# Optimization experiments

Hardware: AMD Instinct MI355X
Metric: run time of the kernel (lower is better)

## Reference

```python
import jax, jax.numpy as jnp
import numpy as np
from jax import lax

NUM_BINS = 64
GROUP = 16
HIDDEN = 128
DOWNSAMPLE = 32
EPS = 1e-6


def _conv2d(x, w, b, pad, groups=1):
    # x: (N, Cin, H, W), w: (Cout, Cin//groups, kh, kw)
    y = lax.conv_general_dilated(
        x, w, window_strides=(1, 1), padding=[(pad, pad), (pad, pad)],
        dimension_numbers=("NCHW", "OIHW", "NCHW"), feature_group_count=groups)
    return y + b[None, :, None, None]


def _lut_net(delta_cdf, w1, b1, w2, b2, w3, b3):
    # MonotonicLUT1D.forward on (1, G, 1, K)
    h = jax.nn.relu(_conv2d(delta_cdf, w1, b1, pad=2))
    h = jax.nn.relu(_conv2d(h, w2, b2, pad=2, groups=HIDDEN))
    d = _conv2d(h, w3, b3, pad=0)
    d = jax.nn.softplus(d)
    cdf = jnp.cumsum(d, axis=-1)
    cdf = cdf / (cdf[..., -1:] + EPS)
    identity = jnp.linspace(0.0, 1.0, NUM_BINS, dtype=cdf.dtype).reshape(1, 1, 1, -1)
    return cdf + identity  # (1, G, 1, K)


def reference(x, w1, b1, w2, b2, w3, b3, alpha):
    B, C, H, W = x.shape
    K, G, ds = NUM_BINS, GROUP, DOWNSAMPLE

    # per-sample, per-channel min-max normalize
    x_min = jnp.min(x, axis=(2, 3), keepdims=True)
    x_max = jnp.max(x, axis=(2, 3), keepdims=True)
    x01 = (x - x_min) / (x_max - x_min + EPS)

    # exact adaptive avg pool to (ds, ds) (H, W divisible by ds)
    x_small = x01.reshape(B, C, ds, H // ds, ds, W // ds).mean(axis=(3, 5))
    x_small = lax.stop_gradient(x_small)  # detach_hist=True

    # histogram CDF estimate (no grad in original)
    x_group = x_small.reshape(B, G, C // G, ds, ds).mean(axis=2)  # (B, G, ds, ds)
    idx = jnp.clip(jnp.round(x_group * (K - 1)).astype(jnp.int32), 0, K - 1)
    idx = idx.reshape(B, G, -1)
    hist = jax.nn.one_hot(idx, K, dtype=jnp.float32).sum(axis=2)  # (B, G, K)
    pdf = hist / (hist.sum(axis=-1, keepdims=True) + EPS)
    cdf = jnp.cumsum(pdf, axis=-1)
    delta_cdf = cdf.mean(axis=0, keepdims=True).reshape(1, G, 1, K).astype(x.dtype)

    adapt_cdf = _lut_net(delta_cdf, w1, b1, w2, b2, w3, b3)  # (1, G, 1, K)

    # per-pixel LUT gather + lerp
    lut = adapt_cdf[0, :, 0, :]                 # (G, K)
    group_ids = jnp.arange(C) // (C // G)
    lut_c = lut[group_ids]                       # (C, K)

    pos = x01 * (K - 1)
    idx_lo = jnp.clip(jnp.floor(pos).astype(jnp.int32), 0, K - 1)
    idx_hi = jnp.clip(idx_lo + 1, 0, K - 1)
    w_hi = (pos - idx_lo).astype(lut.dtype)

    lut_e = jnp.broadcast_to(lut_c[None], (B, C, K))
    v_lo = jnp.take_along_axis(lut_e, idx_lo.reshape(B, C, -1), axis=2)
    v_hi = jnp.take_along_axis(lut_e, idx_hi.reshape(B, C, -1), axis=2)
    x_eq01 = (v_lo + w_hi.reshape(B, C, -1) * (v_hi - v_lo)).reshape(B, C, H, W)

    a = jax.nn.sigmoid(alpha)
    out01 = a * x_eq01 + (1.0 - a) * x01
    return out01 * (x_max - x_min) + x_min


def setup_inputs() -> dict:
    key = jax.random.key(0)
    ks = jax.random.split(key, 8)
    B, C, H, W = 2, 16, 1024, 1024
    x = jax.random.normal(ks[0], (B, C, H, W), dtype=jnp.float32)
    w1 = jax.random.normal(ks[1], (HIDDEN, GROUP, 5, 5), dtype=jnp.float32) * 0.05
    b1 = jnp.zeros((HIDDEN,), dtype=jnp.float32)
    w2 = jax.random.normal(ks[2], (HIDDEN, 1, 5, 5), dtype=jnp.float32) * 0.05
    b2 = jnp.zeros((HIDDEN,), dtype=jnp.float32)
    w3 = jax.random.normal(ks[3], (GROUP, HIDDEN, 1, 1), dtype=jnp.float32) * 0.05
    b3 = jnp.zeros((GROUP,), dtype=jnp.float32)
    alpha = jnp.asarray(0.25, dtype=jnp.float32)
    return {"x": x, "w1": w1, "b1": b1, "w2": w2, "b2": b2, "w3": w3, "b3": b3, "alpha": alpha}
```

## Files before the change

kernel.cpp:

```cpp
#include <hip/hip_runtime.h>
#include <math.h>

#define NBINS   64
#define GROUPS  16
#define HIDDEN  128
#define EPSF    1e-6f

#define IMG_ELEMS   (1024*1024)
#define F4_PER_ROW  256
#define NIMG        32

typedef float nfloat4 __attribute__((ext_vector_type(4)));

__global__ __launch_bounds__(256) void k_stats(
        const float* __restrict__ x,
        float* __restrict__ blocksum,
        float* __restrict__ pmin,
        float* __restrict__ pmax)
{
    const int bid = blockIdx.x;
    const int bc  = bid >> 5;
    const int i   = bid & 31;
    const int t   = threadIdx.x;
    const int lane = t & 63;
    const int wave = t >> 6;

    const float4* xin = (const float4*)(x + (size_t)bc * IMG_ELEMS);
    const int rowbase = (i * 32) * F4_PER_ROW;

    float s = 0.f, mn = INFINITY, mx = -INFINITY;
    #pragma unroll 4
    for (int r = 0; r < 32; ++r) {
        float4 v = xin[rowbase + r * F4_PER_ROW + t];
        s += (v.x + v.y) + (v.z + v.w);
        mn = fminf(mn, fminf(fminf(v.x, v.y), fminf(v.z, v.w)));
        mx = fmaxf(mx, fmaxf(fmaxf(v.x, v.y), fmaxf(v.z, v.w)));
    }

    s += __shfl_xor(s, 4, 64);
    s += __shfl_xor(s, 2, 64);
    s += __shfl_xor(s, 1, 64);
    if ((t & 7) == 0)
        blocksum[bc * 1024 + i * 32 + (t >> 3)] = s;

    #pragma unroll
    for (int st = 32; st > 0; st >>= 1) {
        mn = fminf(mn, __shfl_xor(mn, st, 64));
        mx = fmaxf(mx, __shfl_xor(mx, st, 64));
    }
    __shared__ float wmn[4], wmx[4];
    if (lane == 0) { wmn[wave] = mn; wmx[wave] = mx; }
    __syncthreads();
    if (t == 0) {
        pmin[bid] = fminf(fminf(wmn[0], wmn[1]), fminf(wmn[2], wmn[3]));
        pmax[bid] = fmaxf(fmaxf(wmx[0], wmx[1]), fmaxf(wmx[2], wmx[3]));
    }
}

__global__ __launch_bounds__(256) void k_hist(
        const float* __restrict__ pmin, const float* __restrict__ pmax,
        const float* __restrict__ blocksum,
        float* __restrict__ gmin, float* __restrict__ gmax,
        float* __restrict__ pcdf)
{
    const int bc   = blockIdx.x;
    const int t    = threadIdx.x;
    const int lane = t & 63;
    const int wave = t >> 6;

    __shared__ float s_mn, s_inv;
    if (wave == 0) {
        float mn = (lane < 32) ? pmin[bc * 32 + lane] : INFINITY;
        float mx = (lane < 32) ? pmax[bc * 32 + lane] : -INFINITY;
        #pragma unroll
        for (int st = 32; st > 0; st >>= 1) {
            mn = fminf(mn, __shfl_xor(mn, st, 64));
            mx = fmaxf(mx, __shfl_xor(mx, st, 64));
        }
        if (lane == 0) {
            gmin[bc] = mn; gmax[bc] = mx;
            s_mn = mn; s_inv = 1.0f / (mx - mn + EPSF);
        }
    }
    __syncthreads();
    const float mnv = s_mn;
    const float inv = s_inv;

    int idx0, idx1, idx2, idx3;
    {
        const float* bs = blocksum + bc * 1024;
        #define MKIDX(D, IT) { \
            float bmean = bs[t + (IT)*256] * (1.0f / 1024.0f); \
            float xs = (bmean - mnv) * inv; \
            int id = (int)rintf(xs * 63.0f); \
            D = max(0, min(id, 63)); }
        MKIDX(idx0, 0) MKIDX(idx1, 1) MKIDX(idx2, 2) MKIDX(idx3, 3)
        #undef MKIDX
    }

    int cnt = 0;
    #pragma unroll 1
    for (int b = 0; b < NBINS; ++b) {
        unsigned long long m0 = __ballot(idx0 == b);
        unsigned long long m1 = __ballot(idx1 == b);
        unsigned long long m2 = __ballot(idx2 == b);
        unsigned long long m3 = __ballot(idx3 == b);
        int p = __popcll(m0) + __popcll(m1) + __popcll(m2) + __popcll(m3);
        cnt += (lane == b) ? p : 0;
    }

    __shared__ int whist[4][NBINS];
    whist[wave][lane] = cnt;
    __syncthreads();

    if (t < NBINS) {
        int h = whist[0][t] + whist[1][t] + whist[2][t] + whist[3][t];
        #pragma unroll
        for (int d = 1; d < 64; d <<= 1) {
            int v = __shfl_up(h, d, 64);
            if (t >= d) h += v;
        }
        const float scale = 0.5f / (1024.0f + EPSF);
        pcdf[bc * NBINS + t] = (float)h * scale;
    }
}

__global__ __launch_bounds__(256) void k_conv12(
        const float* __restrict__ pcdf,
        const float* __restrict__ w1, const float* __restrict__ b1,
        const float* __restrict__ w2, const float* __restrict__ b2,
        float* __restrict__ h2)
{
    __shared__ float dcdf[GROUPS][NBINS];
    __shared__ float w1s[4 * GROUPS * 5];
    __shared__ float w2s[4][5];
    __shared__ float h1s[4][NBINS + 4];

    const int t   = threadIdx.x;
    const int ocb = blockIdx.x * 4;
    const int ocl = t >> 6;
    const int k   = t & 63;

    for (int o = t; o < GROUPS * NBINS; o += 256)
        ((float*)dcdf)[o] = pcdf[o] + pcdf[GROUPS * NBINS + o];

    for (int o = t; o < 4 * GROUPS * 5; o += 256) {
        const int oo  = o / 80;
        const int rem = o - oo * 80;
        const int ic  = rem / 5;
        const int tap = rem - ic * 5;
        w1s[o] = w1[((ocb + oo) * GROUPS + ic) * 25 + 10 + tap];
    }
    if (t < 20) w2s[t / 5][t % 5] = w2[(ocb + t / 5) * 25 + 10 + t % 5];
    if (t < 4)  { h1s[t][0] = 0.f; h1s[t][1] = 0.f;
                  h1s[t][NBINS + 2] = 0.f; h1s[t][NBINS + 3] = 0.f; }
    __syncthreads();

    float acc = b1[ocb + ocl];
    const float* wrow = w1s + ocl * 80;
    for (int ic = 0; ic < GROUPS; ++ic) {
        #pragma unroll
        for (int tap = 0; tap < 5; ++tap) {
            const int kk = k - 2 + tap;
            if (kk >= 0 && kk < NBINS)
                acc += wrow[ic * 5 + tap] * dcdf[ic][kk];
        }
    }
    h1s[ocl][k + 2] = fmaxf(acc, 0.f);
    __syncthreads();

    float a = b2[ocb + ocl];
    #pragma unroll
    for (int tap = 0; tap < 5; ++tap)
        a += w2s[ocl][tap] * h1s[ocl][k + tap];
    h2[(ocb + ocl) * NBINS + k] = fmaxf(a, 0.f);
}

__global__ __launch_bounds__(256) void k_tail(
        const float* __restrict__ h2,
        const float* __restrict__ w3, const float* __restrict__ b3,
        float* __restrict__ lut)
{
    __shared__ float h2s[HIDDEN][NBINS];
    __shared__ float w3s[GROUPS * HIDDEN];
    __shared__ float sd[GROUPS][NBINS];
    const int t = threadIdx.x;

    for (int o = t; o < HIDDEN * NBINS; o += 256) ((float*)h2s)[o] = h2[o];
    for (int o = t; o < GROUPS * HIDDEN; o += 256) w3s[o] = w3[o];
    __syncthreads();

    const int k = t & 63;
    const int g0 = t >> 6;
    float acc0 = b3[g0 + 0];
    float acc1 = b3[g0 + 4];
    float acc2 = b3[g0 + 8];
    float acc3 = b3[g0 + 12];
    for (int h = 0; h < HIDDEN; ++h) {
        const float v = h2s[h][k];
        acc0 += w3s[(g0 + 0) * HIDDEN + h] * v;
        acc1 += w3s[(g0 + 4) * HIDDEN + h] * v;
        acc2 += w3s[(g0 + 8) * HIDDEN + h] * v;
        acc3 += w3s[(g0 + 12) * HIDDEN + h] * v;
    }
    #define SOFTPLUS(z) (fmaxf(z, 0.f) + log1pf(expf(-fabsf(z))))
    sd[g0 + 0][k]  = SOFTPLUS(acc0);
    sd[g0 + 4][k]  = SOFTPLUS(acc1);
    sd[g0 + 8][k]  = SOFTPLUS(acc2);
    sd[g0 + 12][k] = SOFTPLUS(acc3);
    #undef SOFTPLUS
    __syncthreads();

    if (t < GROUPS) {
        float run = 0.f;
        for (int kk = 0; kk < NBINS; ++kk) { run += sd[t][kk]; sd[t][kk] = run; }
        const float invn = 1.0f / (run + EPSF);
        for (int kk = 0; kk < NBINS; ++kk)
            lut[t * NBINS + kk] = sd[t][kk] * invn + (float)kk * (1.0f / 63.0f);
    }
}

__device__ __forceinline__ float remap1(float v, float mnv, float inv, float r,
                                        float aa, const float* lut_s)
{
    float x01 = (v - mnv) * inv;
    float pos = x01 * 63.0f;
    int il = (int)floorf(pos);
    il = max(0, min(il, 63));
    const int ih = min(il + 1, 63);
    const float w = pos - (float)il;
    const float vlo = lut_s[il];
    const float vhi = lut_s[ih];
    const float xe = fmaf(w, vhi - vlo, vlo);
    const float o01 = aa * xe + (1.0f - aa) * x01;
    return o01 * r + mnv;
}

__global__ __launch_bounds__(256) void k_apply(
        const float* __restrict__ x,
        const float* __restrict__ gmin, const float* __restrict__ gmax,
        const float* __restrict__ lut, const float* __restrict__ alpha,
        float* __restrict__ out)
{
    const int img  = blockIdx.x >> 6;
    const int part = blockIdx.x & 63;
    const int c    = img & 15;
    const int t    = threadIdx.x;

    __shared__ float lut_s[NBINS];
    if (t < NBINS) lut_s[t] = lut[c * NBINS + t];
    __syncthreads();

    const float mnv = gmin[img];
    const float mxv = gmax[img];
    const float r   = mxv - mnv;
    const float inv = 1.0f / (r + EPSF);
    const float aa  = 1.0f / (1.0f + expf(-alpha[0]));

    const size_t base4 = (size_t)img * (IMG_ELEMS / 4) + (size_t)part * 4096;
    const float4* xin = (const float4*)x;
    nfloat4* o4 = (nfloat4*)out;

    #pragma unroll 2
    for (int it = 0; it < 16; ++it) {
        const size_t f = base4 + (size_t)t + (size_t)it * 256;
        float4 v = xin[f];
        nfloat4 w;
        w.x = remap1(v.x, mnv, inv, r, aa, lut_s);
        w.y = remap1(v.y, mnv, inv, r, aa, lut_s);
        w.z = remap1(v.z, mnv, inv, r, aa, lut_s);
        w.w = remap1(v.w, mnv, inv, r, aa, lut_s);
        __builtin_nontemporal_store(w, &o4[f]);
    }
}

extern "C" void kernel_launch(void* const* d_in, const int* in_sizes, int n_in,
                              void* d_out, int out_size, void* d_ws, size_t ws_size,
                              hipStream_t stream)
{
    const float* x     = (const float*)d_in[0];
    const float* w1    = (const float*)d_in[1];
    const float* b1    = (const float*)d_in[2];
    const float* w2    = (const float*)d_in[3];
    const float* b2    = (const float*)d_in[4];
    const float* w3    = (const float*)d_in[5];
    const float* b3    = (const float*)d_in[6];
    const float* alpha = (const float*)d_in[7];
    float* out = (float*)d_out;

    float* ws = (float*)d_ws;
    float* blocksum = ws;
    float* pmin     = ws + 32768;
    float* pmax     = ws + 33792;
    float* gmin     = ws + 34816;
    float* gmax     = ws + 34848;
    float* lut      = ws + 34880;
    float* pcdf     = ws + 35904;
    float* h2       = ws + 37952;

    k_stats <<<NIMG * 32, 256, 0, stream>>>(x, blocksum, pmin, pmax);
    k_hist  <<<NIMG,      256, 0, stream>>>(pmin, pmax, blocksum, gmin, gmax, pcdf);
    k_conv12<<<32,        256, 0, stream>>>(pcdf, w1, b1, w2, b2, h2);
    k_tail  <<<1,         256, 0, stream>>>(h2, w3, b3, lut);
    k_apply <<<NIMG * 64, 256, 0, stream>>>(x, gmin, gmax, lut, alpha, out);
}
```

Before: 88.03 us.

## Fuse histogram, conv and LUT-tail kernels into one single-block kernel

The three small middle kernels (per-image histogram/CDF, the two conv layers, and the 1x1 conv with softplus/cumsum tail) are merged into one 1024-thread, single-block kernel. Every intermediate (pcdf, h1/h2) now stays in shared memory, which removes two kernel launches and the global round-trips between them. In exchange, work that used to spread across 32 blocks now runs serially on a single CU, including eight sequential histogram iterations per team. The second conv also updates h1 in place within a wave, relying on lockstep execution with no barrier.

Result: slower. 258.3 us, median of 2 (+193.5%).

```diff
diff --git a/kernel.cpp b/kernel.cpp
--- a/kernel.cpp
+++ b/kernel.cpp
@@ -57,158 +57,118 @@
     }
 }
 
-__global__ __launch_bounds__(256) void k_hist(
+__global__ __launch_bounds__(1024) void k_mid(
         const float* __restrict__ pmin, const float* __restrict__ pmax,
         const float* __restrict__ blocksum,
+        const float* __restrict__ w1, const float* __restrict__ b1,
+        const float* __restrict__ w2, const float* __restrict__ b2,
+        const float* __restrict__ w3, const float* __restrict__ b3,
         float* __restrict__ gmin, float* __restrict__ gmax,
-        float* __restrict__ pcdf)
-{
-    const int bc   = blockIdx.x;
+        float* __restrict__ lut)
+{
     const int t    = threadIdx.x;
     const int lane = t & 63;
     const int wave = t >> 6;
 
-    __shared__ float s_mn, s_inv;
-    if (wave == 0) {
-        float mn = (lane < 32) ? pmin[bc * 32 + lane] : INFINITY;
-        float mx = (lane < 32) ? pmax[bc * 32 + lane] : -INFINITY;
+    __shared__ float s_mn[NIMG], s_inv[NIMG];
+    __shared__ float pcdf_l[NIMG][NBINS];
+    __shared__ int   whist[4][4][NBINS];
+    __shared__ float dcdf[GROUPS][NBINS];
+    __shared__ float h1[HIDDEN][NBINS];
+    __shared__ float sd[GROUPS][NBINS];
+
+    {
+        const int pair = t >> 5, j = t & 31;
+        float mn = pmin[pair * 32 + j];
+        float mx = pmax[pair * 32 + j];
         #pragma unroll
-        for (int st = 32; st > 0; st >>= 1) {
+        for (int st = 16; st > 0; st >>= 1) {
             mn = fminf(mn, __shfl_xor(mn, st, 64));
             mx = fmaxf(mx, __shfl_xor(mx, st, 64));
         }
-        if (lane == 0) {
-            gmin[bc] = mn; gmax[bc] = mx;
-            s_mn = mn; s_inv = 1.0f / (mx - mn + EPSF);
-        }
-    }
-    __syncthreads();
-    const float mnv = s_mn;
-    const float inv = s_inv;
-
-    int idx0, idx1, idx2, idx3;
-    {
+        if (j == 0) {
+            gmin[pair] = mn; gmax[pair] = mx;
+            s_mn[pair] = mn; s_inv[pair] = 1.0f / (mx - mn + EPSF);
+        }
+    }
+    __syncthreads();
+
+    const int team = wave >> 2;
+    const int q    = wave & 3;
+    const int lt   = q * 64 + lane;
+    for (int iter = 0; iter < 8; ++iter) {
+        const int bc = team * 8 + iter;
+        const float mnv = s_mn[bc];
+        const float inv = s_inv[bc];
         const float* bs = blocksum + bc * 1024;
-        #define MKIDX(D, IT) { \
-            float bmean = bs[t + (IT)*256] * (1.0f / 1024.0f); \
-            float xs = (bmean - mnv) * inv; \
-            int id = (int)rintf(xs * 63.0f); \
-            D = max(0, min(id, 63)); }
-        MKIDX(idx0, 0) MKIDX(idx1, 1) MKIDX(idx2, 2) MKIDX(idx3, 3)
-        #undef MKIDX
-    }
-
-    int cnt = 0;
-    #pragma unroll 1
-    for (int b = 0; b < NBINS; ++b) {
-        unsigned long long m0 = __ballot(idx0 == b);
-        unsigned long long m1 = __ballot(idx1 == b);
-        unsigned long long m2 = __ballot(idx2 == b);
-        unsigned long long m3 = __ballot(idx3 == b);
-        int p = __popcll(m0) + __popcll(m1) + __popcll(m2) + __popcll(m3);
-        cnt += (lane == b) ? p : 0;
-    }
-
-    __shared__ int whist[4][NBINS];
-    whist[wave][lane] = cnt;
-    __syncthreads();
-
-    if (t < NBINS) {
-        int h = whist[0][t] + whist[1][t] + whist[2][t] + whist[3][t];
+        int idx[4];
         #pragma unroll
-        for (int d = 1; d < 64; d <<= 1) {
-            int v = __shfl_up(h, d, 64);
-            if (t >= d) h += v;
-        }
-        const float scale = 0.5f / (1024.0f + EPSF);
-        pcdf[bc * NBINS + t] = (float)h * scale;
-    }
-}
-
-__global__ __launch_bounds__(256) void k_conv12(
-        const float* __restrict__ pcdf,
-        const float* __restrict__ w1, const float* __restrict__ b1,
-        const float* __restrict__ w2, const float* __restrict__ b2,
-        float* __restrict__ h2)
-{
-    __shared__ float dcdf[GROUPS][NBINS];
-    __shared__ float w1s[4 * GROUPS * 5];
-    __shared__ float w2s[4][5];
-    __shared__ float h1s[4][NBINS + 4];
-
-    const int t   = threadIdx.x;
-    const int ocb = blockIdx.x * 4;
-    const int ocl = t >> 6;
-    const int k   = t & 63;
-
-    for (int o = t; o < GROUPS * NBINS; o += 256)
-        ((float*)dcdf)[o] = pcdf[o] + pcdf[GROUPS * NBINS + o];
-
-    for (int o = t; o < 4 * GROUPS * 5; o += 256) {
-        const int oo  = o / 80;
-        const int rem = o - oo * 80;
-        const int ic  = rem / 5;
-        const int tap = rem - ic * 5;
-        w1s[o] = w1[((ocb + oo) * GROUPS + ic) * 25 + 10 + tap];
-    }
-    if (t < 20) w2s[t / 5][t % 5] = w2[(ocb + t / 5) * 25 + 10 + t % 5];
-    if (t < 4)  { h1s[t][0] = 0.f; h1s[t][1] = 0.f;
-                  h1s[t][NBINS + 2] = 0.f; h1s[t][NBINS + 3] = 0.f; }
-    __syncthreads();
-
-    float acc = b1[ocb + ocl];
-    const float* wrow = w1s + ocl * 80;
-    for (int ic = 0; ic < GROUPS; ++ic) {
+        for (int i = 0; i < 4; ++i) {
+            float bmean = bs[lt + i * 256] * (1.0f / 1024.0f);
+            float xs = (bmean - mnv) * inv;
+            int id = (int)rintf(xs * 63.0f);
+            idx[i] = max(0, min(id, 63));
+        }
+        int cnt = 0;
+        #pragma unroll 1
+        for (int b = 0; b < NBINS; ++b) {
+            int p = __popcll(__ballot(idx[0] == b)) + __popcll(__ballot(idx[1] == b))
+                  + __popcll(__ballot(idx[2] == b)) + __popcll(__ballot(idx[3] == b));
+            cnt += (lane == b) ? p : 0;
+        }
+        whist[team][q][lane] = cnt;
+        __syncthreads();
+        if (q == 0) {
+            int h = whist[team][0][lane] + whist[team][1][lane]
+                  + whist[team][2][lane] + whist[team][3][lane];
+            #pragma unroll
+            for (int d = 1; d < 64; d <<= 1) {
+                int v = __shfl_up(h, d, 64);
+                if (lane >= d) h += v;
+            }
+            pcdf_l[bc][lane] = (float)h * (0.5f / (1024.0f + EPSF));
+        }
+        __syncthreads();
+    }
+
+    dcdf[wave][lane] = pcdf_l[wave][lane] + pcdf_l[GROUPS + wave][lane];
+    __syncthreads();
+
+    for (int i = 0; i < 8; ++i) {
+        const int oc = i * 16 + wave;
+        const int k  = lane;
+        float acc = b1[oc];
+        const float* wp = w1 + (oc * GROUPS) * 25 + 10;
+        for (int ic = 0; ic < GROUPS; ++ic) {
+            const float* wrow = wp + ic * 25;
+            #pragma unroll
+            for (int tap = 0; tap < 5; ++tap) {
+                const int kk = k - 2 + tap;
+                if (kk >= 0 && kk < NBINS)
+                    acc += wrow[tap] * dcdf[ic][kk];
+            }
+        }
+        h1[oc][k] = fmaxf(acc, 0.f);
+        const float* w2p = w2 + oc * 25 + 10;
+        float a = b2[oc];
         #pragma unroll
         for (int tap = 0; tap < 5; ++tap) {
             const int kk = k - 2 + tap;
             if (kk >= 0 && kk < NBINS)
-                acc += wrow[ic * 5 + tap] * dcdf[ic][kk];
-        }
-    }
-    h1s[ocl][k + 2] = fmaxf(acc, 0.f);
-    __syncthreads();
-
-    float a = b2[ocb + ocl];
-    #pragma unroll
-    for (int tap = 0; tap < 5; ++tap)
-        a += w2s[ocl][tap] * h1s[ocl][k + tap];
-    h2[(ocb + ocl) * NBINS + k] = fmaxf(a, 0.f);
-}
-
-__global__ __launch_bounds__(256) void k_tail(
-        const float* __restrict__ h2,
-        const float* __restrict__ w3, const float* __restrict__ b3,
-        float* __restrict__ lut)
-{
-    __shared__ float h2s[HIDDEN][NBINS];
-    __shared__ float w3s[GROUPS * HIDDEN];
-    __shared__ float sd[GROUPS][NBINS];
-    const int t = threadIdx.x;
-
-    for (int o = t; o < HIDDEN * NBINS; o += 256) ((float*)h2s)[o] = h2[o];
-    for (int o = t; o < GROUPS * HIDDEN; o += 256) w3s[o] = w3[o];
-    __syncthreads();
-
-    const int k = t & 63;
-    const int g0 = t >> 6;
-    float acc0 = b3[g0 + 0];
-    float acc1 = b3[g0 + 4];
-    float acc2 = b3[g0 + 8];
-    float acc3 = b3[g0 + 12];
-    for (int h = 0; h < HIDDEN; ++h) {
-        const float v = h2s[h][k];
-        acc0 += w3s[(g0 + 0) * HIDDEN + h] * v;
-        acc1 += w3s[(g0 + 4) * HIDDEN + h] * v;
-        acc2 += w3s[(g0 + 8) * HIDDEN + h] * v;
-        acc3 += w3s[(g0 + 12) * HIDDEN + h] * v;
-    }
-    #define SOFTPLUS(z) (fmaxf(z, 0.f) + log1pf(expf(-fabsf(z))))
-    sd[g0 + 0][k]  = SOFTPLUS(acc0);
-    sd[g0 + 4][k]  = SOFTPLUS(acc1);
-    sd[g0 + 8][k]  = SOFTPLUS(acc2);
-    sd[g0 + 12][k] = SOFTPLUS(acc3);
-    #undef SOFTPLUS
+                a += w2p[tap] * h1[oc][kk];
+        }
+        h1[oc][k] = fmaxf(a, 0.f);
+    }
+    __syncthreads();
+
+    {
+        const int g = wave, k = lane;
+        float acc = b3[g];
+        const float* w3p = w3 + g * HIDDEN;
+        for (int h = 0; h < HIDDEN; ++h)
+            acc += w3p[h] * h1[h][k];
+        sd[g][k] = fmaxf(acc, 0.f) + log1pf(expf(-fabsf(acc)));
+    }
     __syncthreads();
 
     if (t < GROUPS) {
@@ -295,12 +255,10 @@
     float* gmin     = ws + 34816;
     float* gmax     = ws + 34848;
     float* lut      = ws + 34880;
-    float* pcdf     = ws + 35904;
-    float* h2       = ws + 37952;
-
-    k_stats <<<NIMG * 32, 256, 0, stream>>>(x, blocksum, pmin, pmax);
-    k_hist  <<<NIMG,      256, 0, stream>>>(pmin, pmax, blocksum, gmin, gmax, pcdf);
-    k_conv12<<<32,        256, 0, stream>>>(pcdf, w1, b1, w2, b2, h2);
-    k_tail  <<<1,         256, 0, stream>>>(h2, w3, b3, lut);
-    k_apply <<<NIMG * 64, 256, 0, stream>>>(x, gmin, gmax, lut, alpha, out);
-}
+
+    k_stats<<<NIMG * 32, 256,  0, stream>>>(x, blocksum, pmin, pmax);
+    k_mid  <<<1,         1024, 0, stream>>>(pmin, pmax, blocksum,
+                                            w1, b1, w2, b2, w3, b3,
+                                            gmin, gmax, lut);
+    k_apply<<<NIMG * 64, 256,  0, stream>>>(x, gmin, gmax, lut, alpha, out);
+}
```

## Fuse LUT tail into apply kernel and use shuffles for depthwise conv

Applied to the files above, without the earlier changes.

Removes the single-block k_tail kernel by having every k_apply block recompute its channel's 1x1 conv, softplus, cumsum and normalisation into shared memory. The depthwise conv in k_conv12 now reads neighbours through wavefront shuffles instead of a shared buffer and an extra barrier. This saves one serial launch and a low-occupancy kernel on the critical path. In exchange, each of the 2048 apply blocks redoes a 128x64 dot-product reduction plus a shuffle scan before streaming its pixels.

After: 81.93 us. -6.9%, faster.

```diff
diff --git a/kernel.cpp b/kernel.cpp
--- a/kernel.cpp
+++ b/kernel.cpp
@@ -134,7 +134,6 @@
     __shared__ float dcdf[GROUPS][NBINS];
     __shared__ float w1s[4 * GROUPS * 5];
     __shared__ float w2s[4][5];
-    __shared__ float h1s[4][NBINS + 4];
 
     const int t   = threadIdx.x;
     const int ocb = blockIdx.x * 4;
@@ -152,8 +151,6 @@
         w1s[o] = w1[((ocb + oo) * GROUPS + ic) * 25 + 10 + tap];
     }
     if (t < 20) w2s[t / 5][t % 5] = w2[(ocb + t / 5) * 25 + 10 + t % 5];
-    if (t < 4)  { h1s[t][0] = 0.f; h1s[t][1] = 0.f;
-                  h1s[t][NBINS + 2] = 0.f; h1s[t][NBINS + 3] = 0.f; }
     __syncthreads();
 
     float acc = b1[ocb + ocl];
@@ -166,89 +163,61 @@
                 acc += wrow[ic * 5 + tap] * dcdf[ic][kk];
         }
     }
-    h1s[ocl][k + 2] = fmaxf(acc, 0.f);
-    __syncthreads();
-
+    const float c1 = fmaxf(acc, 0.f);
+
+    const float m2 = __shfl_up(c1, 2, 64);
+    const float m1 = __shfl_up(c1, 1, 64);
+    const float p1 = __shfl_down(c1, 1, 64);
+    const float p2 = __shfl_down(c1, 2, 64);
     float a = b2[ocb + ocl];
-    #pragma unroll
-    for (int tap = 0; tap < 5; ++tap)
-        a += w2s[ocl][tap] * h1s[ocl][k + tap];
+    a += w2s[ocl][0] * ((k >= 2) ? m2 : 0.f);
+    a += w2s[ocl][1] * ((k >= 1) ? m1 : 0.f);
+    a += w2s[ocl][2] * c1;
+    a += w2s[ocl][3] * ((k <= 62) ? p1 : 0.f);
+    a += w2s[ocl][4] * ((k <= 61) ? p2 : 0.f);
     h2[(ocb + ocl) * NBINS + k] = fmaxf(a, 0.f);
-}
-
-__global__ __launch_bounds__(256) void k_tail(
-        const float* __restrict__ h2,
-        const float* __restrict__ w3, const float* __restrict__ b3,
-        float* __restrict__ lut)
-{
-    __shared__ float h2s[HIDDEN][NBINS];
-    __shared__ float w3s[GROUPS * HIDDEN];
-    __shared__ float sd[GROUPS][NBINS];
-    const int t = threadIdx.x;
-
-    for (int o = t; o < HIDDEN * NBINS; o += 256) ((float*)h2s)[o] = h2[o];
-    for (int o = t; o < GROUPS * HIDDEN; o += 256) w3s[o] = w3[o];
-    __syncthreads();
-
-    const int k = t & 63;
-    const int g0 = t >> 6;
-    float acc0 = b3[g0 + 0];
-    float acc1 = b3[g0 + 4];
-    float acc2 = b3[g0 + 8];
-    float acc3 = b3[g0 + 12];
-    for (int h = 0; h < HIDDEN; ++h) {
-        const float v = h2s[h][k];
-        acc0 += w3s[(g0 + 0) * HIDDEN + h] * v;
-        acc1 += w3s[(g0 + 4) * HIDDEN + h] * v;
-        acc2 += w3s[(g0 + 8) * HIDDEN + h] * v;
-        acc3 += w3s[(g0 + 12) * HIDDEN + h] * v;
-    }
-    #define SOFTPLUS(z) (fmaxf(z, 0.f) + log1pf(expf(-fabsf(z))))
-    sd[g0 + 0][k]  = SOFTPLUS(acc0);
-    sd[g0 + 4][k]  = SOFTPLUS(acc1);
-    sd[g0 + 8][k]  = SOFTPLUS(acc2);
-    sd[g0 + 12][k] = SOFTPLUS(acc3);
-    #undef SOFTPLUS
-    __syncthreads();
-
-    if (t < GROUPS) {
-        float run = 0.f;
-        for (int kk = 0; kk < NBINS; ++kk) { run += sd[t][kk]; sd[t][kk] = run; }
-        const float invn = 1.0f / (run + EPSF);
-        for (int kk = 0; kk < NBINS; ++kk)
-            lut[t * NBINS + kk] = sd[t][kk] * invn + (float)kk * (1.0f / 63.0f);
-    }
-}
-
-__device__ __forceinline__ float remap1(float v, float mnv, float inv, float r,
-                                        float aa, const float* lut_s)
-{
-    float x01 = (v - mnv) * inv;
-    float pos = x01 * 63.0f;
-    int il = (int)floorf(pos);
-    il = max(0, min(il, 63));
-    const int ih = min(il + 1, 63);
-    const float w = pos - (float)il;
-    const float vlo = lut_s[il];
-    const float vhi = lut_s[ih];
-    const float xe = fmaf(w, vhi - vlo, vlo);
-    const float o01 = aa * xe + (1.0f - aa) * x01;
-    return o01 * r + mnv;
 }
 
 __global__ __launch_bounds__(256) void k_apply(
         const float* __restrict__ x,
         const float* __restrict__ gmin, const float* __restrict__ gmax,
-        const float* __restrict__ lut, const float* __restrict__ alpha,
+        const float* __restrict__ h2,
+        const float* __restrict__ w3, const float* __restrict__ b3,
+        const float* __restrict__ alpha,
         float* __restrict__ out)
 {
     const int img  = blockIdx.x >> 6;
     const int part = blockIdx.x & 63;
     const int c    = img & 15;
     const int t    = threadIdx.x;
-
+    const int q    = t >> 6;
+    const int k    = t & 63;
+
+    __shared__ float partial[4][NBINS];
     __shared__ float lut_s[NBINS];
-    if (t < NBINS) lut_s[t] = lut[c * NBINS + t];
+
+    {
+        float part_acc = 0.f;
+        const float* w3p = w3 + c * HIDDEN + q * 32;
+        const float* h2p = h2 + (q * 32) * NBINS + k;
+        #pragma unroll 8
+        for (int h = 0; h < 32; ++h)
+            part_acc += w3p[h] * h2p[h * NBINS];
+        partial[q][k] = part_acc;
+    }
+    __syncthreads();
+    if (q == 0) {
+        float acc = b3[c] + ((partial[0][k] + partial[1][k])
+                           + (partial[2][k] + partial[3][k]));
+        float d = fmaxf(acc, 0.f) + log1pf(expf(-fabsf(acc)));
+        #pragma unroll
+        for (int dd = 1; dd < 64; dd <<= 1) {
+            float v = __shfl_up(d, dd, 64);
+            if (k >= dd) d += v;
+        }
+        const float tot = __shfl(d, 63, 64);
+        lut_s[k] = d / (tot + EPSF) + (float)k * (1.0f / 63.0f);
+    }
     __syncthreads();
 
     const float mnv = gmin[img];
@@ -266,10 +235,42 @@
         const size_t f = base4 + (size_t)t + (size_t)it * 256;
         float4 v = xin[f];
         nfloat4 w;
-        w.x = remap1(v.x, mnv, inv, r, aa, lut_s);
-        w.y = remap1(v.y, mnv, inv, r, aa, lut_s);
-        w.z = remap1(v.z, mnv, inv, r, aa, lut_s);
-        w.w = remap1(v.w, mnv, inv, r, aa, lut_s);
+        {
+            float x01 = (v.x - mnv) * inv;
+            float pos = x01 * 63.0f;
+            int il = max(0, min((int)floorf(pos), 63));
+            int ih = min(il + 1, 63);
+            float wt = pos - (float)il;
+            float vlo = lut_s[il], vhi = lut_s[ih];
+            w.x = (aa * fmaf(wt, vhi - vlo, vlo) + (1.0f - aa) * x01) * r + mnv;
+        }
+        {
+            float x01 = (v.y - mnv) * inv;
+            float pos = x01 * 63.0f;
+            int il = max(0, min((int)floorf(pos), 63));
+            int ih = min(il + 1, 63);
+            float wt = pos - (float)il;
+            float vlo = lut_s[il], vhi = lut_s[ih];
+            w.y = (aa * fmaf(wt, vhi - vlo, vlo) + (1.0f - aa) * x01) * r + mnv;
+        }
+        {
+            float x01 = (v.z - mnv) * inv;
+            float pos = x01 * 63.0f;
+            int il = max(0, min((int)floorf(pos), 63));
+            int ih = min(il + 1, 63);
+            float wt = pos - (float)il;
+            float vlo = lut_s[il], vhi = lut_s[ih];
+            w.z = (aa * fmaf(wt, vhi - vlo, vlo) + (1.0f - aa) * x01) * r + mnv;
+        }
+        {
+            float x01 = (v.w - mnv) * inv;
+            float pos = x01 * 63.0f;
+            int il = max(0, min((int)floorf(pos), 63));
+            int ih = min(il + 1, 63);
+            float wt = pos - (float)il;
+            float vlo = lut_s[il], vhi = lut_s[ih];
+            w.w = (aa * fmaf(wt, vhi - vlo, vlo) + (1.0f - aa) * x01) * r + mnv;
+        }
         __builtin_nontemporal_store(w, &o4[f]);
     }
 }
@@ -294,13 +295,11 @@
     float* pmax     = ws + 33792;
     float* gmin     = ws + 34816;
     float* gmax     = ws + 34848;
-    float* lut      = ws + 34880;
-    float* pcdf     = ws + 35904;
-    float* h2       = ws + 37952;
+    float* pcdf     = ws + 34880;
+    float* h2       = ws + 36928;
 
     k_stats <<<NIMG * 32, 256, 0, stream>>>(x, blocksum, pmin, pmax);
     k_hist  <<<NIMG,      256, 0, stream>>>(pmin, pmax, blocksum, gmin, gmax, pcdf);
     k_conv12<<<32,        256, 0, stream>>>(pcdf, w1, b1, w2, b2, h2);
-    k_tail  <<<1,         256, 0, stream>>>(h2, w3, b3, lut);
-    k_apply <<<NIMG * 64, 256, 0, stream>>>(x, gmin, gmax, lut, alpha, out);
-}
+    k_apply <<<NIMG * 64, 256, 0, stream>>>(x, gmin, gmax, h2, w3, b3, alpha, out);
+}
```
